# Performance work log

Measured on AMD Instinct MI355X. Metric: run time of the kernel, lower is better.

Reference implementation:

```python
import jax, jax.numpy as jnp
import numpy as np

B, T, V, E, H, F, A, P = 128, 24, 10000, 512, 512, 2048, 512, 196


def setup_inputs() -> dict:
    key = jax.random.key(0)
    ks = jax.random.split(key, 16)
    rn = lambda k, shape, s=0.02: jax.random.normal(k, shape, jnp.float32) * s
    return dict(
        features=jax.random.normal(ks[0], (B, P, F), jnp.float32),
        captions=jax.random.randint(ks[1], (B, T), 0, V),
        emb=rn(ks[2], (V, E)),
        att_Wf=rn(ks[3], (F, A)), att_bf=jnp.zeros((A,), jnp.float32),
        att_Wh=rn(ks[4], (H, A)), att_bh=jnp.zeros((A,), jnp.float32),
        att_v=rn(ks[5], (A,)), att_bv=jnp.zeros((), jnp.float32),
        proj_W=rn(ks[6], (F, H)), proj_b=jnp.zeros((H,), jnp.float32),
        W_ih0=rn(ks[7], (4 * H, E + H)), W_hh0=rn(ks[8], (4 * H, H)),
        b_ih0=jnp.zeros((4 * H,), jnp.float32), b_hh0=jnp.zeros((4 * H,), jnp.float32),
        W_ih1=rn(ks[9], (4 * H, H)), W_hh1=rn(ks[10], (4 * H, H)),
        b_ih1=jnp.zeros((4 * H,), jnp.float32), b_hh1=jnp.zeros((4 * H,), jnp.float32),
        ln_g=jnp.ones((H,), jnp.float32), ln_b=jnp.zeros((H,), jnp.float32),
        skip_W=rn(ks[11], (E + 2 * H, H)), skip_b=jnp.zeros((H,), jnp.float32),
        fc_W=rn(ks[12], (H, V)), fc_b=jnp.zeros((V,), jnp.float32),
    )


def _lstm_cell(x, h, c, W_ih, W_hh, b_ih, b_hh):
    # PyTorch gate order: i, f, g, o
    g = x @ W_ih.T + b_ih + h @ W_hh.T + b_hh
    i, f, gg, o = jnp.split(g, 4, axis=-1)
    c2 = jax.nn.sigmoid(f) * c + jax.nn.sigmoid(i) * jnp.tanh(gg)
    h2 = jax.nn.sigmoid(o) * jnp.tanh(c2)
    return h2, c2


def reference(features, captions, emb, att_Wf, att_bf, att_Wh, att_bh, att_v,
              att_bv, proj_W, proj_b, W_ih0, W_hh0, b_ih0, b_hh0, W_ih1, W_hh1,
              b_ih1, b_hh1, ln_g, ln_b, skip_W, skip_b, fc_W, fc_b):
    embs = emb[captions]                       # [B, T, E] (dropout = identity, eval mode)
    feat_att = features @ att_Wf + att_bf      # [B, P, A] precomputed once

    def step(carry, emb_t):
        h0, c0, h1, c1 = carry
        # additive attention driven by top-layer hidden h1
        e = jnp.tanh(feat_att + (h1 @ att_Wh + att_bh)[:, None, :])  # [B, P, A]
        scores = e @ att_v + att_bv                                  # [B, P]
        alpha = jax.nn.softmax(scores, axis=-1)
        ctx = jnp.einsum('bp,bpf->bf', alpha, features)              # [B, F]
        ctx = jax.nn.relu(ctx @ proj_W + proj_b)                     # [B, H]
        x = jnp.concatenate([emb_t, ctx], axis=-1)                   # [B, E+H]
        h0n, c0n = _lstm_cell(x, h0, c0, W_ih0, W_hh0, b_ih0, b_hh0)
        h1n, c1n = _lstm_cell(h0n, h1, c1, W_ih1, W_hh1, b_ih1, b_hh1)
        skip = jnp.concatenate([h1n, x], axis=-1) @ skip_W + skip_b  # [B, H]
        mu = skip.mean(-1, keepdims=True)
        var = ((skip - mu) ** 2).mean(-1, keepdims=True)
        ln = (skip - mu) / jnp.sqrt(var + 1e-5) * ln_g + ln_b
        out = ln @ fc_W + fc_b                                       # [B, V]
        return (h0n, c0n, h1n, c1n), out

    init = tuple(jnp.zeros((B, H), jnp.float32) for _ in range(4))
    _, outs = jax.lax.scan(step, init, jnp.swapaxes(embs, 0, 1))     # [T, B, V]
    return jnp.swapaxes(outs, 0, 1)                                  # [B, T, V]
```

## Files before the change

### kernel.cpp

```cpp
#include <hip/hip_runtime.h>
#include <hip/hip_bf16.h>
#include <math.h>

constexpr int Bb = 128, Tt = 24, Vv = 10000, Ee = 512, Hh = 512, Ff = 2048, Aa = 512, Pp = 196;
constexpr int XS = Ee + 2 * Hh;
constexpr int NFC = 10112;

typedef __attribute__((ext_vector_type(8))) short bhalf8;
typedef __attribute__((ext_vector_type(4))) float fx4;

__device__ __forceinline__ ushort f2bf(float f) {
    __hip_bfloat16 h = __float2bfloat16(f);
    return *reinterpret_cast<ushort*>(&h);
}
__device__ __forceinline__ float bf2f(ushort u) {
    __hip_bfloat16 h = *reinterpret_cast<__hip_bfloat16*>(&u);
    return __bfloat162float(h);
}
__device__ __forceinline__ float sigm_(float x) { return 1.f / (1.f + __expf(-x)); }
__device__ __forceinline__ float tanh_(float x) {
    x = fminf(fmaxf(x, -15.f), 15.f);
    float e = __expf(2.f * x);
    return (e - 1.f) / (e + 1.f);
}

__device__ __forceinline__ void gld_lds16(const void* g, void* l) {
    __builtin_amdgcn_global_load_lds(
        (const __attribute__((address_space(1))) unsigned int*)g,
        (__attribute__((address_space(3))) unsigned int*)l, 16, 0, 0);
}

template<bool AFP32, int OUT_MODE, int SWZ>
__global__ __launch_bounds__(256) void mfma_gemm_staged(
    const void* __restrict__ Av, int lda,
    const ushort* __restrict__ B, int ldb, int K,
    const float* __restrict__ bias1, const float* __restrict__ bias2,
    void* __restrict__ Cv, int ldc, int N)
{
    __shared__ __align__(16) ushort Alds[128 * 32];
    __shared__ __align__(16) ushort Blds[128 * 32];

    const int tid = threadIdx.x;
    const int lane = tid & 63, wave = tid >> 6;
    const int row16 = lane & 15, quad = lane >> 4;
    const int wm = wave >> 1, wn = wave & 1;

    int lm, ln;
    {
        const int nx = gridDim.x, ny = gridDim.y;
        const int flat = blockIdx.y * nx + blockIdx.x;
        const int total = nx * ny;
        if ((total & 7) == 0) {
            const int T = (flat & 7) * (total >> 3) + (flat >> 3);
            if (SWZ == 1) { ln = T / ny; lm = T - ln * ny; }
            else          { lm = T / nx; ln = T - lm * nx; }
        } else { lm = blockIdx.y; ln = blockIdx.x; }
    }
    const int n0 = ln * 128, m0 = lm * 128;

    const int sr = tid >> 2, sc = (tid & 3) * 8;

    const ushort* A16s0 = nullptr; const ushort* A16s1 = nullptr;
    const float*  A32s0 = nullptr; const float*  A32s1 = nullptr;
    if (AFP32) {
        A32s0 = (const float*)Av + (size_t)(m0 + sr) * lda + sc;
        A32s1 = (const float*)Av + (size_t)(m0 + 64 + sr) * lda + sc;
    } else {
        A16s0 = (const ushort*)Av + (size_t)(m0 + sr) * lda + sc;
        A16s1 = (const ushort*)Av + (size_t)(m0 + 64 + sr) * lda + sc;
    }
    const ushort* Bs0 = B + (size_t)(n0 + sr) * ldb + sc;
    const ushort* Bs1 = B + (size_t)(n0 + 64 + sr) * ldb + sc;
    ushort* Ad0 = Alds + sr * 32 + sc;
    ushort* Ad1 = Alds + (64 + sr) * 32 + sc;
    ushort* Bd0 = Blds + sr * 32 + sc;
    ushort* Bd1 = Blds + (64 + sr) * 32 + sc;

    const ushort* Afr = Alds + (wm * 64 + row16) * 32 + quad * 8;
    const ushort* Bfr = Blds + (wn * 64 + row16) * 32 + quad * 8;

    fx4 acc[4][4] = {};

    for (int k0 = 0; k0 < K; k0 += 32) {
        if (AFP32) {
            fx4 u0 = *(const fx4*)(A32s0 + k0);
            fx4 u1 = *(const fx4*)(A32s0 + k0 + 4);
            fx4 u2 = *(const fx4*)(A32s1 + k0);
            fx4 u3 = *(const fx4*)(A32s1 + k0 + 4);
            bhalf8 v0, v1;
#pragma unroll
            for (int j = 0; j < 4; ++j) {
                v0[j] = (short)f2bf(u0[j]); v0[4 + j] = (short)f2bf(u1[j]);
                v1[j] = (short)f2bf(u2[j]); v1[4 + j] = (short)f2bf(u3[j]);
            }
            *(bhalf8*)Ad0 = v0;
            *(bhalf8*)Ad1 = v1;
        } else {
            gld_lds16(A16s0 + k0, Ad0);
            gld_lds16(A16s1 + k0, Ad1);
        }
        gld_lds16(Bs0 + k0, Bd0);
        gld_lds16(Bs1 + k0, Bd1);
        __syncthreads();

        bhalf8 af[4], bfv[4];
#pragma unroll
        for (int f = 0; f < 4; ++f) {
            af[f]  = *(const bhalf8*)(Afr + f * 16 * 32);
            bfv[f] = *(const bhalf8*)(Bfr + f * 16 * 32);
        }
#pragma unroll
        for (int i = 0; i < 4; ++i)
#pragma unroll
            for (int j = 0; j < 4; ++j)
                acc[i][j] = __builtin_amdgcn_mfma_f32_16x16x32_bf16(af[i], bfv[j], acc[i][j], 0, 0, 0);
        __syncthreads();
    }

#pragma unroll
    for (int j = 0; j < 4; ++j) {
        const int col = n0 + wn * 64 + j * 16 + row16;
        if (OUT_MODE == 2 && col >= N) continue;
        const float badd = (bias1 ? bias1[col] : 0.f) + (bias2 ? bias2[col] : 0.f);
#pragma unroll
        for (int i = 0; i < 4; ++i) {
            const int mb = m0 + wm * 64 + i * 16 + quad * 4;
#pragma unroll
            for (int r = 0; r < 4; ++r) {
                const int m = mb + r;
                const float v = acc[i][j][r] + badd;
                if (OUT_MODE == 0)      ((float*)Cv)[(size_t)m * ldc + col] = v;
                else if (OUT_MODE == 1) ((ushort*)Cv)[(size_t)m * ldc + col] = f2bf(v);
                else { int t = m >> 7, b = m & 127; ((float*)Cv)[((size_t)(b * Tt + t)) * Vv + col] = v; }
            }
        }
    }
}

template<bool HAS_PRE>
__global__ __launch_bounds__(256) void gates_cell_ksplit(
    const ushort* __restrict__ A1, int lda1, const ushort* __restrict__ B1,
    const ushort* __restrict__ A2, const ushort* __restrict__ B2,
    const float* __restrict__ pre,
    const float* __restrict__ bias_a, const float* __restrict__ bias_b,
    float* __restrict__ cstate,
    ushort* __restrict__ hout,
    ushort* __restrict__ xs_slot)
{
    __shared__ float part[4][4][4][64];
    const int tid = threadIdx.x, lane = tid & 63, wave = tid >> 6;
    const int row16 = lane & 15, quad = lane >> 4;
    const int m0 = blockIdx.x * 16;
    const int j0 = blockIdx.y * 16;
    const int mat = wave >> 1, klo = (wave & 1) * 256;

    const ushort* Abase = mat ? A2 : A1;
    const int lda = mat ? Hh : lda1;
    const ushort* ap = Abase + (size_t)(m0 + row16) * lda + klo + quad * 8;
    const ushort* Bsel = mat ? B2 : B1;
    const ushort* bp[4];
#pragma unroll
    for (int f = 0; f < 4; ++f)
        bp[f] = Bsel + (size_t)(f * Hh + j0 + row16) * Hh + klo + quad * 8;

    fx4 acc[4] = {};
#pragma unroll 2
    for (int k0 = 0; k0 < 256; k0 += 32) {
        bhalf8 a = *(const bhalf8*)(ap + k0);
#pragma unroll
        for (int f = 0; f < 4; ++f)
            acc[f] = __builtin_amdgcn_mfma_f32_16x16x32_bf16(a, *(const bhalf8*)(bp[f] + k0), acc[f], 0, 0, 0);
    }
#pragma unroll
    for (int f = 0; f < 4; ++f)
#pragma unroll
        for (int r = 0; r < 4; ++r)
            part[wave][f][r][lane] = acc[f][r];
    __syncthreads();

    const int r = wave;
    const int j = j0 + row16;
    const int b = m0 + quad * 4 + r;
    float g4[4];
#pragma unroll
    for (int f = 0; f < 4; ++f)
        g4[f] = part[0][f][r][lane] + part[1][f][r][lane]
              + part[2][f][r][lane] + part[3][f][r][lane];
    float gi = g4[0], gf = g4[1], gg = g4[2], go = g4[3];
    if (HAS_PRE) {
        const float* pr = pre + (size_t)b * (4 * Hh) + j;
        gi += pr[0]; gf += pr[Hh]; gg += pr[2 * Hh]; go += pr[3 * Hh];
    } else {
        gi += bias_a[j] + bias_b[j];
        gf += bias_a[Hh + j] + bias_b[Hh + j];
        gg += bias_a[2 * Hh + j] + bias_b[2 * Hh + j];
        go += bias_a[3 * Hh + j] + bias_b[3 * Hh + j];
    }
    const int idx = b * Hh + j;
    float c = sigm_(gf) * cstate[idx] + sigm_(gi) * tanh_(gg);
    cstate[idx] = c;
    float h = sigm_(go) * tanh_(c);
    hout[idx] = f2bf(h);
    if (xs_slot) xs_slot[(size_t)b * XS + j] = f2bf(h);
}

__global__ __launch_bounds__(1024) void att_scores_kernel(
    const ushort* __restrict__ featfp,
    const ushort* __restrict__ h1cur,
    const ushort* __restrict__ attWh_t,
    const float* __restrict__ att_bh, const float* __restrict__ att_v,
    const float* __restrict__ att_bv,
    float* __restrict__ scores_g)
{
    __shared__ float h1s[Hh];
    __shared__ float kpart[2][Aa];
    __shared__ float atth[Aa];
    const int b = blockIdx.x >> 1, ph = blockIdx.x & 1;
    const int tid = threadIdx.x, lane = tid & 63, wave = tid >> 6;

    if (tid < Hh) h1s[tid] = bf2f(h1cur[b * Hh + tid]);
    __syncthreads();

    {
        const int a = tid & 511, kh = tid >> 9;
        const ushort* wr = attWh_t + (size_t)a * Hh + kh * 256;
        const float* hp = h1s + kh * 256;
        float s = 0.f;
#pragma unroll 4
        for (int k0 = 0; k0 < 256; k0 += 8) {
            bhalf8 w = *(const bhalf8*)(wr + k0);
#pragma unroll
            for (int jj = 0; jj < 8; ++jj) s += hp[k0 + jj] * bf2f((ushort)w[jj]);
        }
        kpart[kh][a] = s;
    }
    __syncthreads();
    if (tid < Aa) atth[tid] = kpart[0][tid] + kpart[1][tid] + att_bh[tid];
    __syncthreads();

    float attv8[8], atth8[8];
#pragma unroll
    for (int jj = 0; jj < 8; ++jj) { attv8[jj] = att_v[lane * 8 + jj]; atth8[jj] = atth[lane * 8 + jj]; }
    const ushort* fa = featfp + (size_t)b * Pp * 1024;
    const int pend = ph * 98 + 98;
    for (int p = ph * 98 + wave; p < pend; p += 16) {
        bhalf8 v = *(const bhalf8*)(fa + (size_t)p * 1024 + lane * 8);
        float partial = 0.f;
#pragma unroll
        for (int jj = 0; jj < 8; ++jj) partial += tanh_(bf2f((ushort)v[jj]) + atth8[jj]) * attv8[jj];
#pragma unroll
        for (int o = 32; o > 0; o >>= 1) partial += __shfl_down(partial, o);
        if (lane == 0) scores_g[b * 256 + p] = partial + att_bv[0];
    }
}

__global__ __launch_bounds__(1024) void att_pv_kernel(
    const ushort* __restrict__ featfp,
    const float* __restrict__ scores_g,
    const float* __restrict__ proj_b,
    ushort* __restrict__ xs_t)
{
    __shared__ float scs[200];
    __shared__ float part[4][256];
    const int b = blockIdx.x >> 1, hh = blockIdx.x & 1;
    const int tid = threadIdx.x, lane = tid & 63;

    if (tid < Pp) scs[tid] = scores_g[b * 256 + tid];
    __syncthreads();

    if (tid < 64) {
        float m = -1e30f;
        for (int p = lane; p < Pp; p += 64) m = fmaxf(m, scs[p]);
#pragma unroll
        for (int o = 32; o > 0; o >>= 1) m = fmaxf(m, __shfl_down(m, o));
        m = __shfl(m, 0);
        float s = 0.f;
        for (int p = lane; p < Pp; p += 64) { float e = __expf(scs[p] - m); scs[p] = e; s += e; }
#pragma unroll
        for (int o = 32; o > 0; o >>= 1) s += __shfl_down(s, o);
        s = __shfl(s, 0);
        float inv = 1.f / s;
        for (int p = lane; p < Pp; p += 64) scs[p] *= inv;
    }
    __syncthreads();

    const int hl = tid & 255, pq = tid >> 8;
    const int h = hh * 256 + hl;
    const ushort* fpx = featfp + (size_t)b * Pp * 1024 + 512 + h;
    float s = 0.f;
    const int p1 = pq * 49 + 49;
#pragma unroll 4
    for (int p = pq * 49; p < p1; ++p) s += scs[p] * bf2f(fpx[(size_t)p * 1024]);
    part[pq][hl] = s;
    __syncthreads();
    if (tid < 256) {
        float v = part[0][tid] + part[1][tid] + part[2][tid] + part[3][tid] + proj_b[hh * 256 + tid];
        xs_t[(size_t)b * XS + Ee + Hh + hh * 256 + tid] = f2bf(fmaxf(v, 0.f));
    }
}

__global__ __launch_bounds__(256) void transpose_f32_bf16(
    const float* __restrict__ in, ushort* __restrict__ out, int R, int C)
{
    __shared__ float tile[32][33];
    const int tx = threadIdx.x & 31, ty = threadIdx.x >> 5;
    const int c0 = blockIdx.x * 32, r0 = blockIdx.y * 32;
    for (int i = ty; i < 32; i += 8) {
        int r = r0 + i, c = c0 + tx;
        tile[i][tx] = (r < R && c < C) ? in[(size_t)r * C + c] : 0.f;
    }
    __syncthreads();
    for (int i = ty; i < 32; i += 8) {
        int oc = c0 + i, orr = r0 + tx;
        if (oc < C && orr < R) out[(size_t)oc * R + orr] = f2bf(tile[tx][i]);
    }
}

__global__ __launch_bounds__(256) void convert_slice_kernel(
    const float* __restrict__ in, int inld, int c0,
    ushort* __restrict__ out, int R, int C)
{
    int idx = blockIdx.x * 256 + threadIdx.x;
    if (idx >= R * C) return;
    int r = idx / C, c = idx - r * C;
    out[idx] = f2bf(in[(size_t)r * inld + c0 + c]);
}

__global__ __launch_bounds__(256) void emb_fill_kernel(
    const float* __restrict__ emb, const int* __restrict__ captions,
    ushort* __restrict__ xs)
{
    int idx = blockIdx.x * 256 + threadIdx.x;
    if (idx >= Tt * Bb * Ee) return;
    int e = idx % Ee, rb = idx / Ee;
    int t = rb / Bb, b = rb % Bb;
    int tok = captions[b * Tt + t];
    xs[((size_t)(t * Bb + b)) * XS + Ee + e] = f2bf(emb[(size_t)tok * Ee + e]);
}

__global__ __launch_bounds__(256) void layernorm_kernel(
    const float* __restrict__ x, const float* __restrict__ g,
    const float* __restrict__ beta, ushort* __restrict__ y)
{
    __shared__ float red[4];
    const int row = blockIdx.x;
    const float* xr = x + (size_t)row * Hh;
    const int tid = threadIdx.x, lane = tid & 63, wave = tid >> 6;
    float v0 = xr[tid], v1 = xr[tid + 256];
    float s = v0 + v1;
#pragma unroll
    for (int o = 32; o > 0; o >>= 1) s += __shfl_down(s, o);
    if (lane == 0) red[wave] = s;
    __syncthreads();
    float mu = (red[0] + red[1] + red[2] + red[3]) / 512.f;
    float d0 = v0 - mu, d1 = v1 - mu;
    float q = d0 * d0 + d1 * d1;
#pragma unroll
    for (int o = 32; o > 0; o >>= 1) q += __shfl_down(q, o);
    __syncthreads();
    if (lane == 0) red[wave] = q;
    __syncthreads();
    float var = (red[0] + red[1] + red[2] + red[3]) / 512.f;
    float inv = 1.f / sqrtf(var + 1e-5f);
    y[(size_t)row * Hh + tid]       = f2bf(d0 * inv * g[tid] + beta[tid]);
    y[(size_t)row * Hh + tid + 256] = f2bf(d1 * inv * g[tid + 256] + beta[tid + 256]);
}

extern "C" void kernel_launch(void* const* d_in, const int* in_sizes, int n_in,
                              void* d_out, int out_size, void* d_ws, size_t ws_size,
                              hipStream_t stream)
{
    const float* features = (const float*)d_in[0];
    const int*   captions = (const int*)d_in[1];
    const float* emb      = (const float*)d_in[2];
    const float* att_Wf   = (const float*)d_in[3];
    const float* att_bf   = (const float*)d_in[4];
    const float* att_Wh   = (const float*)d_in[5];
    const float* att_bh   = (const float*)d_in[6];
    const float* att_v    = (const float*)d_in[7];
    const float* att_bv   = (const float*)d_in[8];
    const float* proj_W   = (const float*)d_in[9];
    const float* proj_b   = (const float*)d_in[10];
    const float* W_ih0    = (const float*)d_in[11];
    const float* W_hh0    = (const float*)d_in[12];
    const float* b_ih0    = (const float*)d_in[13];
    const float* b_hh0    = (const float*)d_in[14];
    const float* W_ih1    = (const float*)d_in[15];
    const float* W_hh1    = (const float*)d_in[16];
    const float* b_ih1    = (const float*)d_in[17];
    const float* b_hh1    = (const float*)d_in[18];
    const float* ln_g     = (const float*)d_in[19];
    const float* ln_b     = (const float*)d_in[20];
    const float* skip_W   = (const float*)d_in[21];
    const float* skip_b   = (const float*)d_in[22];
    const float* fc_W     = (const float*)d_in[23];
    const float* fc_b     = (const float*)d_in[24];

    char* base = (char*)d_ws;
    size_t off = 0;
    auto alloc = [&](size_t bytes) { char* p = base + off; off = (off + bytes + 255) & ~(size_t)255; return p; };

    float*  c0      = (float*)alloc(Bb * Hh * 4);
    float*  c1      = (float*)alloc(Bb * Hh * 4);
    ushort* h0b[2]  = {(ushort*)alloc(Bb * Hh * 2), (ushort*)alloc(Bb * Hh * 2)};
    ushort* h1b[2]  = {(ushort*)alloc(Bb * Hh * 2), (ushort*)alloc(Bb * Hh * 2)};
    size_t state_bytes = off;

    ushort* attWf_t  = (ushort*)alloc((size_t)Aa * Ff * 2);
    ushort* projW_t  = (ushort*)alloc((size_t)Hh * Ff * 2);
    ushort* attWh_t  = (ushort*)alloc((size_t)Aa * Hh * 2);
    ushort* skipW_t  = (ushort*)alloc((size_t)Hh * XS * 2);
    ushort* fcW_t    = (ushort*)alloc((size_t)NFC * Hh * 2);
    ushort* Wemb0    = (ushort*)alloc((size_t)4 * Hh * Ee * 2);
    ushort* Wctx0    = (ushort*)alloc((size_t)4 * Hh * Hh * 2);
    ushort* Whh0     = (ushort*)alloc((size_t)4 * Hh * Hh * 2);
    ushort* Wih1     = (ushort*)alloc((size_t)4 * Hh * Hh * 2);
    ushort* Whh1     = (ushort*)alloc((size_t)4 * Hh * Hh * 2);
    ushort* featfp   = (ushort*)alloc((size_t)Bb * Pp * 1024 * 2);
    ushort* xs       = (ushort*)alloc((size_t)Tt * Bb * XS * 2);
    float*  g0pre    = (float*)alloc((size_t)Tt * Bb * 4 * Hh * 4);
    float*  skip_pre = (float*)alloc((size_t)Tt * Bb * Hh * 4);
    ushort* ln_all   = (ushort*)alloc((size_t)Tt * Bb * Hh * 2);
    float*  bias_cat = (float*)alloc(1024 * 4);
    float*  scores_g = (float*)alloc((size_t)Bb * 256 * 4);

    hipMemsetAsync(d_ws, 0, state_bytes, stream);
    hipMemsetAsync(fcW_t + (size_t)Vv * Hh, 0, (size_t)(NFC - Vv) * Hh * 2, stream);
    hipMemsetAsync(bias_cat, 0, 1024 * 4, stream);
    hipMemcpyAsync(bias_cat, att_bf, Aa * 4, hipMemcpyDeviceToDevice, stream);

    dim3 blk(256);

    transpose_f32_bf16<<<dim3(Aa / 32, Ff / 32), blk, 0, stream>>>(att_Wf, attWf_t, Ff, Aa);
    transpose_f32_bf16<<<dim3(Hh / 32, Ff / 32), blk, 0, stream>>>(proj_W, projW_t, Ff, Hh);
    transpose_f32_bf16<<<dim3(Aa / 32, Hh / 32), blk, 0, stream>>>(att_Wh, attWh_t, Hh, Aa);
    transpose_f32_bf16<<<dim3(Hh / 32, XS / 32), blk, 0, stream>>>(skip_W, skipW_t, XS, Hh);
    transpose_f32_bf16<<<dim3((Vv + 31) / 32, Hh / 32), blk, 0, stream>>>(fc_W, fcW_t, Hh, Vv);
    int nW = 4 * Hh * Hh;
    convert_slice_kernel<<<(nW + 255) / 256, blk, 0, stream>>>(W_ih0, Ee + Hh, 0,  Wemb0, 4 * Hh, Ee);
    convert_slice_kernel<<<(nW + 255) / 256, blk, 0, stream>>>(W_ih0, Ee + Hh, Ee, Wctx0, 4 * Hh, Hh);
    convert_slice_kernel<<<(nW + 255) / 256, blk, 0, stream>>>(W_hh0, Hh, 0, Whh0, 4 * Hh, Hh);
    convert_slice_kernel<<<(nW + 255) / 256, blk, 0, stream>>>(W_ih1, Hh, 0, Wih1, 4 * Hh, Hh);
    convert_slice_kernel<<<(nW + 255) / 256, blk, 0, stream>>>(W_hh1, Hh, 0, Whh1, 4 * Hh, Hh);

    emb_fill_kernel<<<(Tt * Bb * Ee + 255) / 256, blk, 0, stream>>>(emb, captions, xs);

    mfma_gemm_staged<true, 1, 0><<<dim3(1024 / 128, Bb * Pp / 128), blk, 0, stream>>>(
        features, Ff, attWf_t, Ff, Ff, bias_cat, nullptr, featfp, 1024, 1024);

    mfma_gemm_staged<false, 0, 0><<<dim3(4 * Hh / 128, Tt * Bb / 128), blk, 0, stream>>>(
        xs + Ee, XS, Wemb0, Ee, Ee, b_ih0, b_hh0, g0pre, 4 * Hh, 4 * Hh);

    int cur0 = 0, cur1 = 0;
    for (int t = 0; t < Tt; ++t) {
        ushort* xs_t = xs + (size_t)t * Bb * XS;

        att_scores_kernel<<<2 * Bb, dim3(1024), 0, stream>>>(
            featfp, h1b[cur1], attWh_t, att_bh, att_v, att_bv, scores_g);

        att_pv_kernel<<<2 * Bb, dim3(1024), 0, stream>>>(
            featfp, scores_g, proj_b, xs_t);

        gates_cell_ksplit<true><<<dim3(8, 32), blk, 0, stream>>>(
            xs_t + Ee + Hh, XS, Wctx0,
            h0b[cur0], Whh0,
            g0pre + (size_t)t * Bb * 4 * Hh, nullptr, nullptr,
            c0, h0b[cur0 ^ 1], nullptr);

        gates_cell_ksplit<false><<<dim3(8, 32), blk, 0, stream>>>(
            h0b[cur0 ^ 1], Hh, Wih1,
            h1b[cur1], Whh1,
            nullptr, b_ih1, b_hh1,
            c1, h1b[cur1 ^ 1], xs_t);
        cur0 ^= 1; cur1 ^= 1;
    }

    mfma_gemm_staged<false, 0, 0><<<dim3(Hh / 128, Tt * Bb / 128), blk, 0, stream>>>(
        xs, XS, skipW_t, XS, XS, skip_b, nullptr, skip_pre, Hh, Hh);

    layernorm_kernel<<<Tt * Bb, blk, 0, stream>>>(skip_pre, ln_g, ln_b, ln_all);

    mfma_gemm_staged<false, 2, 1><<<dim3(NFC / 128, Tt * Bb / 128), blk, 0, stream>>>(
        ln_all, Hh, fcW_t, Hh, Hh, fc_b, nullptr, (float*)d_out, Vv, Vv);
}
```

Baseline: 2.492 ms.

## Fuse attention score and context kernels; pre-convert features to bf16 before GEMM

Merges the per-step attention score and softmax/context kernels into one kernel. Each of the two blocks per batch row now recomputes all 196 scores locally instead of splitting them and passing them through global memory. This removes one launch and a global round-trip per timestep, at the cost of duplicating the score work. It also batches the five LSTM weight conversions into one launch and, when workspace allows, converts features to bf16 in a vectorized pass so the feature GEMM reads bf16 instead of fp32. That adds an extra full pass over the features.

```diff
diff --git a/kernel.cpp b/kernel.cpp
--- a/kernel.cpp
+++ b/kernel.cpp
@@ -8,6 +8,7 @@
 
 typedef __attribute__((ext_vector_type(8))) short bhalf8;
 typedef __attribute__((ext_vector_type(4))) float fx4;
+typedef __attribute__((ext_vector_type(8))) short short8;
 
 __device__ __forceinline__ ushort f2bf(float f) {
     __hip_bfloat16 h = __float2bfloat16(f);
@@ -204,18 +205,20 @@
     if (xs_slot) xs_slot[(size_t)b * XS + j] = f2bf(h);
 }
 
-__global__ __launch_bounds__(1024) void att_scores_kernel(
+__global__ __launch_bounds__(1024) void attention_fused_kernel(
     const ushort* __restrict__ featfp,
     const ushort* __restrict__ h1cur,
     const ushort* __restrict__ attWh_t,
     const float* __restrict__ att_bh, const float* __restrict__ att_v,
-    const float* __restrict__ att_bv,
-    float* __restrict__ scores_g)
+    const float* __restrict__ att_bv, const float* __restrict__ proj_b,
+    ushort* __restrict__ xs_t)
 {
     __shared__ float h1s[Hh];
     __shared__ float kpart[2][Aa];
     __shared__ float atth[Aa];
-    const int b = blockIdx.x >> 1, ph = blockIdx.x & 1;
+    __shared__ float scs[200];
+    __shared__ float part[4][256];
+    const int b = blockIdx.x >> 1, hh = blockIdx.x & 1;
     const int tid = threadIdx.x, lane = tid & 63, wave = tid >> 6;
 
     if (tid < Hh) h1s[tid] = bf2f(h1cur[b * Hh + tid]);
@@ -242,30 +245,15 @@
 #pragma unroll
     for (int jj = 0; jj < 8; ++jj) { attv8[jj] = att_v[lane * 8 + jj]; atth8[jj] = atth[lane * 8 + jj]; }
     const ushort* fa = featfp + (size_t)b * Pp * 1024;
-    const int pend = ph * 98 + 98;
-    for (int p = ph * 98 + wave; p < pend; p += 16) {
+    for (int p = wave; p < Pp; p += 16) {
         bhalf8 v = *(const bhalf8*)(fa + (size_t)p * 1024 + lane * 8);
         float partial = 0.f;
 #pragma unroll
         for (int jj = 0; jj < 8; ++jj) partial += tanh_(bf2f((ushort)v[jj]) + atth8[jj]) * attv8[jj];
 #pragma unroll
         for (int o = 32; o > 0; o >>= 1) partial += __shfl_down(partial, o);
-        if (lane == 0) scores_g[b * 256 + p] = partial + att_bv[0];
-    }
-}
-
-__global__ __launch_bounds__(1024) void att_pv_kernel(
-    const ushort* __restrict__ featfp,
-    const float* __restrict__ scores_g,
-    const float* __restrict__ proj_b,
-    ushort* __restrict__ xs_t)
-{
-    __shared__ float scs[200];
-    __shared__ float part[4][256];
-    const int b = blockIdx.x >> 1, hh = blockIdx.x & 1;
-    const int tid = threadIdx.x, lane = tid & 63;
-
-    if (tid < Pp) scs[tid] = scores_g[b * 256 + tid];
+        if (lane == 0) scs[p] = partial + att_bv[0];
+    }
     __syncthreads();
 
     if (tid < 64) {
@@ -316,14 +304,39 @@
     }
 }
 
-__global__ __launch_bounds__(256) void convert_slice_kernel(
-    const float* __restrict__ in, int inld, int c0,
-    ushort* __restrict__ out, int R, int C)
-{
+__global__ __launch_bounds__(256) void convert5_kernel(
+    const float* __restrict__ W_ih0, const float* __restrict__ W_hh0,
+    const float* __restrict__ W_ih1, const float* __restrict__ W_hh1,
+    ushort* __restrict__ Wemb0, ushort* __restrict__ Wctx0,
+    ushort* __restrict__ Whh0, ushort* __restrict__ Wih1,
+    ushort* __restrict__ Whh1)
+{
+    const float* in; int ld, c0; ushort* out;
+    switch (blockIdx.y) {
+        case 0:  in = W_ih0; ld = Ee + Hh; c0 = 0;  out = Wemb0; break;
+        case 1:  in = W_ih0; ld = Ee + Hh; c0 = Ee; out = Wctx0; break;
+        case 2:  in = W_hh0; ld = Hh;      c0 = 0;  out = Whh0;  break;
+        case 3:  in = W_ih1; ld = Hh;      c0 = 0;  out = Wih1;  break;
+        default: in = W_hh1; ld = Hh;      c0 = 0;  out = Whh1;  break;
+    }
     int idx = blockIdx.x * 256 + threadIdx.x;
-    if (idx >= R * C) return;
-    int r = idx / C, c = idx - r * C;
-    out[idx] = f2bf(in[(size_t)r * inld + c0 + c]);
+    if (idx >= 4 * Hh * 512) return;
+    int r = idx >> 9, c = idx & 511;
+    out[idx] = f2bf(in[(size_t)r * ld + c0 + c]);
+}
+
+__global__ __launch_bounds__(256) void convert_bulk_kernel(
+    const float* __restrict__ in, ushort* __restrict__ out, long n)
+{
+    long stride = (long)gridDim.x * 256 * 8;
+    for (long i = ((long)blockIdx.x * 256 + threadIdx.x) * 8; i < n; i += stride) {
+        fx4 u0 = *(const fx4*)(in + i);
+        fx4 u1 = *(const fx4*)(in + i + 4);
+        short8 v;
+#pragma unroll
+        for (int j = 0; j < 4; ++j) { v[j] = (short)f2bf(u0[j]); v[4 + j] = (short)f2bf(u1[j]); }
+        *(short8*)(out + i) = v;
+    }
 }
 
 __global__ __launch_bounds__(256) void emb_fill_kernel(
@@ -422,7 +435,11 @@
     float*  skip_pre = (float*)alloc((size_t)Tt * Bb * Hh * 4);
     ushort* ln_all   = (ushort*)alloc((size_t)Tt * Bb * Hh * 2);
     float*  bias_cat = (float*)alloc(1024 * 4);
-    float*  scores_g = (float*)alloc((size_t)Bb * 256 * 4);
+
+    const long nfeat = (long)Bb * Pp * Ff;
+    const size_t featbytes = (size_t)nfeat * 2;
+    bool use_conv = (off + featbytes + 256) <= ws_size;
+    ushort* feat16 = use_conv ? (ushort*)alloc(featbytes) : nullptr;
 
     hipMemsetAsync(d_ws, 0, state_bytes, stream);
     hipMemsetAsync(fcW_t + (size_t)Vv * Hh, 0, (size_t)(NFC - Vv) * Hh * 2, stream);
@@ -436,17 +453,19 @@
     transpose_f32_bf16<<<dim3(Aa / 32, Hh / 32), blk, 0, stream>>>(att_Wh, attWh_t, Hh, Aa);
     transpose_f32_bf16<<<dim3(Hh / 32, XS / 32), blk, 0, stream>>>(skip_W, skipW_t, XS, Hh);
     transpose_f32_bf16<<<dim3((Vv + 31) / 32, Hh / 32), blk, 0, stream>>>(fc_W, fcW_t, Hh, Vv);
-    int nW = 4 * Hh * Hh;
-    convert_slice_kernel<<<(nW + 255) / 256, blk, 0, stream>>>(W_ih0, Ee + Hh, 0,  Wemb0, 4 * Hh, Ee);
-    convert_slice_kernel<<<(nW + 255) / 256, blk, 0, stream>>>(W_ih0, Ee + Hh, Ee, Wctx0, 4 * Hh, Hh);
-    convert_slice_kernel<<<(nW + 255) / 256, blk, 0, stream>>>(W_hh0, Hh, 0, Whh0, 4 * Hh, Hh);
-    convert_slice_kernel<<<(nW + 255) / 256, blk, 0, stream>>>(W_ih1, Hh, 0, Wih1, 4 * Hh, Hh);
-    convert_slice_kernel<<<(nW + 255) / 256, blk, 0, stream>>>(W_hh1, Hh, 0, Whh1, 4 * Hh, Hh);
+    convert5_kernel<<<dim3((4 * Hh * 512 + 255) / 256, 5), blk, 0, stream>>>(
+        W_ih0, W_hh0, W_ih1, W_hh1, Wemb0, Wctx0, Whh0, Wih1, Whh1);
 
     emb_fill_kernel<<<(Tt * Bb * Ee + 255) / 256, blk, 0, stream>>>(emb, captions, xs);
 
-    mfma_gemm_staged<true, 1, 0><<<dim3(1024 / 128, Bb * Pp / 128), blk, 0, stream>>>(
-        features, Ff, attWf_t, Ff, Ff, bias_cat, nullptr, featfp, 1024, 1024);
+    if (use_conv) {
+        convert_bulk_kernel<<<2048, blk, 0, stream>>>(features, feat16, nfeat);
+        mfma_gemm_staged<false, 1, 0><<<dim3(1024 / 128, Bb * Pp / 128), blk, 0, stream>>>(
+            feat16, Ff, attWf_t, Ff, Ff, bias_cat, nullptr, featfp, 1024, 1024);
+    } else {
+        mfma_gemm_staged<true, 1, 0><<<dim3(1024 / 128, Bb * Pp / 128), blk, 0, stream>>>(
+            features, Ff, attWf_t, Ff, Ff, bias_cat, nullptr, featfp, 1024, 1024);
+    }
 
     mfma_gemm_staged<false, 0, 0><<<dim3(4 * Hh / 128, Tt * Bb / 128), blk, 0, stream>>>(
         xs + Ee, XS, Wemb0, Ee, Ee, b_ih0, b_hh0, g0pre, 4 * Hh, 4 * Hh);
@@ -455,11 +474,8 @@
     for (int t = 0; t < Tt; ++t) {
         ushort* xs_t = xs + (size_t)t * Bb * XS;
 
-        att_scores_kernel<<<2 * Bb, dim3(1024), 0, stream>>>(
-            featfp, h1b[cur1], attWh_t, att_bh, att_v, att_bv, scores_g);
-
-        att_pv_kernel<<<2 * Bb, dim3(1024), 0, stream>>>(
-            featfp, scores_g, proj_b, xs_t);
+        attention_fused_kernel<<<2 * Bb, dim3(1024), 0, stream>>>(
+            featfp, h1b[cur1], attWh_t, att_bh, att_v, att_bv, proj_b, xs_t);
 
         gates_cell_ksplit<true><<<dim3(8, 32), blk, 0, stream>>>(
             xs_t + Ee + Hh, XS, Wctx0,
```

After: 2.645 ms. 1.06x slower.
